# Performance work log

Hardware: AMD Instinct MI355X
Metric: run time of the kernel (lower is better)

The kernel has to match this reference:

```python
import jax, jax.numpy as jnp
import numpy as np

N, D, H = 24, 256, 8
F = D // H  # 32


def setup_inputs() -> dict:
    key = jax.random.key(0)
    ks = jax.random.split(key, 9)
    T = 8192
    x = jax.random.normal(ks[0], (T, N * D), dtype=jnp.float32)
    s = 0.02
    # Joint-specific query weights: (H, N, D, F); shared K/V: (H, D, F)
    Wq = jax.random.normal(ks[1], (H, N, D, F), dtype=jnp.float32) * s
    bq = jax.random.normal(ks[2], (H, N, F), dtype=jnp.float32) * s
    Wk = jax.random.normal(ks[3], (H, D, F), dtype=jnp.float32) * s
    bk = jax.random.normal(ks[4], (H, F), dtype=jnp.float32) * s
    Wv = jax.random.normal(ks[5], (H, D, F), dtype=jnp.float32) * s
    bv = jax.random.normal(ks[6], (H, F), dtype=jnp.float32) * s
    gamma = jnp.ones((N * D,), dtype=jnp.float32)
    beta = jnp.zeros((N * D,), dtype=jnp.float32)
    return {"x": x, "Wq": Wq, "bq": bq, "Wk": Wk, "bk": bk,
            "Wv": Wv, "bv": bv, "gamma": gamma, "beta": beta}


def reference(x, Wq, bq, Wk, bk, Wv, bv, gamma, beta):
    T = x.shape[0]
    xr = x.reshape(T, N, D)                                   # (T, N, D)
    # Shared K/V per head, joint-specific Q per head
    k = jnp.einsum('tnd,hdf->thnf', xr, Wk) + bk[None, :, None, :]
    v = jnp.einsum('tnd,hdf->thnf', xr, Wv) + bv[None, :, None, :]
    q = jnp.einsum('tnd,hndf->thnf', xr, Wq) + bq[None, :, :, :]
    scores = jnp.einsum('thnf,thmf->thnm', q, k) / jnp.sqrt(jnp.float32(F))
    attn = jax.nn.softmax(scores, axis=-1)                    # (T, H, N, N)
    out = jnp.einsum('thnm,thmf->thnf', attn, v)              # (T, H, N, F)
    # Concat heads -> (T, N, H*F) = (T, N, D)
    out = jnp.transpose(out, (0, 2, 1, 3)).reshape(T, N * D)
    # Dropout is identity in eval mode; residual + LayerNorm over N*D
    y = x + out
    mu = jnp.mean(y, axis=-1, keepdims=True)
    var = jnp.mean((y - mu) ** 2, axis=-1, keepdims=True)
    y = (y - mu) * jax.lax.rsqrt(var + 1e-5)
    return y * gamma + beta
```

## Files before the change

kernel.cpp:

```cpp
#include <hip/hip_runtime.h>

#define NT 8192
#define NJ 24
#define DD 256
#define NH 8
#define FF 32
#define C3 768

typedef __attribute__((ext_vector_type(8))) _Float16 f16x8;
typedef __attribute__((ext_vector_type(2))) _Float16 half2v;
typedef __attribute__((ext_vector_type(4))) float f32x4;

__device__ __forceinline__ unsigned short f2h(float f) {
    union { _Float16 h; unsigned short u; } c;
    c.h = (_Float16)f;
    return c.u;
}

__device__ __forceinline__ float dot2(unsigned int a, unsigned int b, float c) {
#if __has_builtin(__builtin_amdgcn_fdot2)
    return __builtin_amdgcn_fdot2(__builtin_bit_cast(half2v, a),
                                  __builtin_bit_cast(half2v, b), c, false);
#else
    half2v ha = __builtin_bit_cast(half2v, a);
    half2v hb = __builtin_bit_cast(half2v, b);
    return c + (float)ha[0] * (float)hb[0] + (float)ha[1] * (float)hb[1];
#endif
}

__device__ __forceinline__ void gload16(const void* g, void* l) {
    __builtin_amdgcn_global_load_lds(
        (const __attribute__((address_space(1))) unsigned int*)g,
        (__attribute__((address_space(3))) unsigned int*)l, 16, 0, 0);
}

__global__ __launch_bounds__(256)
void pack_wb(const float* __restrict__ Wq, const float* __restrict__ Wk,
             const float* __restrict__ Wv, unsigned short* __restrict__ wbt,
             const float* __restrict__ bq, const float* __restrict__ bk,
             const float* __restrict__ bv, float* __restrict__ bias) {
    const int b = blockIdx.x;
    const int tid = threadIdx.x;

    if (b < 208) {
        const float* src;
        int n0, nrep, crow0;
        if (b < 192) {
            int h = b / 24, n = b % 24;
            src = Wq + (size_t)(h * NJ + n) * (DD * FF);
            n0 = n; nrep = 1; crow0 = h * FF;
        } else if (b < 200) {
            int h = b - 192;
            src = Wk + (size_t)h * (DD * FF);
            n0 = 0; nrep = NJ; crow0 = 256 + h * FF;
        } else {
            int h = b - 200;
            src = Wv + (size_t)h * (DD * FF);
            n0 = 0; nrep = NJ; crow0 = 512 + h * FF;
        }
        __shared__ unsigned short T[32][264];
        #pragma unroll
        for (int it = 0; it < 4; ++it) {
            int e = (it * 256 + tid) * 8;
            int d = e >> 5;
            int f = e & 31;
            float4 v0 = *(const float4*)(src + e);
            float4 v1 = *(const float4*)(src + e + 4);
            T[f + 0][d] = f2h(v0.x); T[f + 1][d] = f2h(v0.y);
            T[f + 2][d] = f2h(v0.z); T[f + 3][d] = f2h(v0.w);
            T[f + 4][d] = f2h(v1.x); T[f + 5][d] = f2h(v1.y);
            T[f + 6][d] = f2h(v1.z); T[f + 7][d] = f2h(v1.w);
        }
        __syncthreads();
        for (int rep = 0; rep < nrep; ++rep) {
            int n = n0 + rep;
            unsigned short* dst = wbt + ((size_t)n * C3 + crow0) * DD;
            #pragma unroll
            for (int it = 0; it < 4; ++it) {
                int q = it * 256 + tid;
                int r = q >> 5;
                int c8 = (q & 31) * 8;
                *(int4*)(dst + r * DD + c8) = *(const int4*)&T[r][c8];
            }
        }
    } else {
        int idx = (b - 208) * 256 + tid;
        int cb = idx % C3;
        int nb2 = idx / C3;
        float bvv;
        if (cb < 256) {
            int h = cb >> 5, f = cb & 31;
            bvv = bq[((h * NJ + nb2) * FF) + f];
        } else if (cb < 512) {
            int cc = cb - 256; int h = cc >> 5, f = cc & 31;
            bvv = bk[h * FF + f];
        } else {
            int cc = cb - 512; int h = cc >> 5, f = cc & 31;
            bvv = bv[h * FF + f];
        }
        bias[idx] = bvv;
    }
}

#define BM 128
#define BN 128

__global__ __launch_bounds__(256, 3)
void gemm_qkv(const float* __restrict__ x, const unsigned short* __restrict__ wbt,
              const float* __restrict__ bias, unsigned short* __restrict__ qkv,
              int t0, int mbs) {
    const int nwg = gridDim.x;
    const int cpx = nwg >> 3;
    const int bid = blockIdx.x;
    const int swz = (bid & 7) * cpx + (bid >> 3);
    const int nb = swz % 6;
    const int rest = swz / 6;
    const int mb = rest % mbs;
    const int nj = rest / mbs;

    const int tid = threadIdx.x;
    const int wave = tid >> 6, lane = tid & 63;

    __shared__ unsigned short As[BM * 64];
    __shared__ unsigned short Bs[BN * 64];

    f32x4 acc[4][4];
    #pragma unroll
    for (int i = 0; i < 4; ++i)
        #pragma unroll
        for (int j = 0; j < 4; ++j)
            #pragma unroll
            for (int r = 0; r < 4; ++r) acc[i][j][r] = 0.f;

    const int trow0 = t0 + mb * BM;
    const float* srcA = x + (size_t)trow0 * (NJ * DD) + nj * DD;
    const char* srcB = (const char*)(wbt + ((size_t)nj * C3 + (size_t)nb * BN) * DD);

    const int rg = lane >> 3;
    const int sc = (lane & 7) ^ rg;

    const int wr = (wave >> 1) * 64;
    const int wc = (wave & 1) * 64;
    const int lr = lane & 15;
    const int g  = lane >> 4;

    float4 pa[4][2];
    const float* aptr[4];
    #pragma unroll
    for (int it = 0; it < 4; ++it) {
        int q = it * 256 + tid;
        int row = q >> 3;
        int c16 = q & 7;
        aptr[it] = srcA + (size_t)row * (NJ * DD) + c16 * 8;
    }

    #pragma unroll
    for (int it = 0; it < 4; ++it) {
        pa[it][0] = *(const float4*)(aptr[it]);
        pa[it][1] = *(const float4*)(aptr[it] + 4);
    }

    for (int kb = 0; kb < 4; ++kb) {
        #pragma unroll
        for (int i = 0; i < 4; ++i) {
            int row0 = wave * 32 + i * 8;
            gload16(srcB + (size_t)(row0 + rg) * (DD * 2) + kb * 128 + sc * 16,
                    (char*)Bs + row0 * 128);
        }
        #pragma unroll
        for (int it = 0; it < 4; ++it) {
            int q = it * 256 + tid;
            int row = q >> 3;
            int c16 = q & 7;
            float4 v0 = pa[it][0];
            float4 v1 = pa[it][1];
            f16x8 hv;
            hv[0] = (_Float16)v0.x; hv[1] = (_Float16)v0.y;
            hv[2] = (_Float16)v0.z; hv[3] = (_Float16)v0.w;
            hv[4] = (_Float16)v1.x; hv[5] = (_Float16)v1.y;
            hv[6] = (_Float16)v1.z; hv[7] = (_Float16)v1.w;
            int c16s = c16 ^ (row & 7);
            *(f16x8*)((char*)As + row * 128 + c16s * 16) = hv;
        }
        __syncthreads();

        if (kb < 3) {
            #pragma unroll
            for (int it = 0; it < 4; ++it) {
                const float* p = aptr[it] + (kb + 1) * 64;
                pa[it][0] = *(const float4*)p;
                pa[it][1] = *(const float4*)(p + 4);
            }
        }

        #pragma unroll
        for (int kk = 0; kk < 2; ++kk) {
            f16x8 a[4], b[4];
            #pragma unroll
            for (int i = 0; i < 4; ++i) {
                int row = wr + i * 16 + lr;
                int c16 = (kk * 4 + g) ^ (row & 7);
                a[i] = *(const f16x8*)((const char*)As + row * 128 + c16 * 16);
            }
            #pragma unroll
            for (int j = 0; j < 4; ++j) {
                int row = wc + j * 16 + lr;
                int c16 = (kk * 4 + g) ^ (row & 7);
                b[j] = *(const f16x8*)((const char*)Bs + row * 128 + c16 * 16);
            }
            #pragma unroll
            for (int i = 0; i < 4; ++i)
                #pragma unroll
                for (int j = 0; j < 4; ++j)
                    acc[i][j] = __builtin_amdgcn_mfma_f32_16x16x32_f16(a[i], b[j], acc[i][j], 0, 0, 0);
        }
        __syncthreads();
    }

    const int ln = lane & 15;
    const int lq = (lane >> 4) * 4;
    float bv[4];
    #pragma unroll
    for (int j = 0; j < 4; ++j)
        bv[j] = bias[nj * C3 + nb * BN + wc + j * 16 + ln];
    #pragma unroll
    for (int i = 0; i < 4; ++i) {
        #pragma unroll
        for (int r = 0; r < 4; ++r) {
            int trow = mb * BM + wr + i * 16 + lq + r;
            size_t base = ((size_t)trow * NJ + nj) * C3 + (size_t)nb * BN;
            #pragma unroll
            for (int j = 0; j < 4; ++j) {
                float val = acc[i][j][r] + bv[j];
                qkv[base + wc + j * 16 + ln] = f2h(val);
            }
        }
    }
}

__global__ __launch_bounds__(256, 6)
void attn_ln(const unsigned short* __restrict__ qkv, const float* __restrict__ x,
             const float* __restrict__ gamma, const float* __restrict__ beta,
             float* __restrict__ out, int t0) {
    const int tloc = blockIdx.x;
    const int t = t0 + tloc;
    const int tid = threadIdx.x;
    const int wave = tid >> 6, lane = tid & 63;

    __shared__ __align__(16) unsigned short kv[NJ * 512];
    __shared__ float red[8];
    __shared__ float stats[2];
    float4* os4 = (float4*)kv;

    const uint4* tok = (const uint4*)(qkv + (size_t)tloc * (NJ * C3));

    #pragma unroll
    for (int j = 0; j < 6; ++j) {
        int idx = tid + j * 256;
        int m = idx >> 6, r = idx & 63;
        ((uint4*)kv)[(m << 6) + r] = tok[m * 96 + 32 + r];
    }

    const bool active = tid < NH * NJ;
    const int h = active ? (tid / NJ) : 0;
    const int n = active ? (tid - h * NJ) : 0;
    unsigned int qp[16];
    if (active) {
        const uint4* qsrc = tok + n * 96 + h * 4;
        #pragma unroll
        for (int jj = 0; jj < 4; ++jj) {
            uint4 w = qsrc[jj];
            qp[jj * 4 + 0] = w.x; qp[jj * 4 + 1] = w.y;
            qp[jj * 4 + 2] = w.z; qp[jj * 4 + 3] = w.w;
        }
    }
    __syncthreads();

    half2v o2[16];
    if (active) {
        const unsigned short* kbase = kv + h * FF;
        float s[NJ];
        float mx = -1e30f;
        #pragma unroll
        for (int m = 0; m < NJ; ++m) {
            const uint4* kp = (const uint4*)(kbase + m * 512);
            float a = 0.f;
            #pragma unroll
            for (int jj = 0; jj < 4; ++jj) {
                uint4 kw = kp[jj];
                a = dot2(kw.x, qp[jj * 4 + 0], a);
                a = dot2(kw.y, qp[jj * 4 + 1], a);
                a = dot2(kw.z, qp[jj * 4 + 2], a);
                a = dot2(kw.w, qp[jj * 4 + 3], a);
            }
            a *= 0.17677669529663687f;
            s[m] = a;
            mx = fmaxf(mx, a);
        }
        float sum = 0.f;
        #pragma unroll
        for (int m = 0; m < NJ; ++m) { s[m] = __expf(s[m] - mx); sum += s[m]; }
        float inv = 1.f / sum;
        #pragma unroll
        for (int k = 0; k < 16; ++k) o2[k] = half2v{(_Float16)0.f, (_Float16)0.f};
        const unsigned short* vbase = kv + 256 + h * FF;
        #pragma unroll
        for (int m = 0; m < NJ; ++m) {
            float wm = s[m] * inv;
            half2v wv = __builtin_bit_cast(half2v, __builtin_amdgcn_cvt_pkrtz(wm, wm));
            const uint4* vp = (const uint4*)(vbase + m * 512);
            #pragma unroll
            for (int jj = 0; jj < 4; ++jj) {
                uint4 vw = vp[jj];
                o2[jj * 4 + 0] += __builtin_bit_cast(half2v, vw.x) * wv;
                o2[jj * 4 + 1] += __builtin_bit_cast(half2v, vw.y) * wv;
                o2[jj * 4 + 2] += __builtin_bit_cast(half2v, vw.z) * wv;
                o2[jj * 4 + 3] += __builtin_bit_cast(half2v, vw.w) * wv;
            }
        }
    }
    __syncthreads();
    if (active) {
        int base4 = n * 64 + h * 8;
        #pragma unroll
        for (int jj = 0; jj < 8; ++jj) {
            int wi = base4 + jj;
            int sw = wi ^ ((wi >> 6) & 7);
            os4[sw] = make_float4((float)o2[jj * 2][0], (float)o2[jj * 2][1],
                                  (float)o2[jj * 2 + 1][0], (float)o2[jj * 2 + 1][1]);
        }
    }
    __syncthreads();

    const float4* x4 = (const float4*)(x + (size_t)t * (NJ * DD));
    float4 yv[6];
    float sum = 0.f, sq = 0.f;
    #pragma unroll
    for (int j = 0; j < 6; ++j) {
        int ri = tid + j * 256;
        float4 a = x4[ri];
        float4 b = os4[ri ^ ((ri >> 6) & 7)];
        float4 y;
        y.x = a.x + b.x; y.y = a.y + b.y; y.z = a.z + b.z; y.w = a.w + b.w;
        yv[j] = y;
        sum += y.x + y.y + y.z + y.w;
        sq  += y.x * y.x + y.y * y.y + y.z * y.z + y.w * y.w;
    }
    #pragma unroll
    for (int off = 32; off > 0; off >>= 1) {
        sum += __shfl_down(sum, off);
        sq  += __shfl_down(sq, off);
    }
    if (lane == 0) { red[wave] = sum; red[4 + wave] = sq; }
    __syncthreads();
    if (tid == 0) {
        float s = red[0] + red[1] + red[2] + red[3];
        float q = red[4] + red[5] + red[6] + red[7];
        float mu = s * (1.f / 6144.f);
        float var = q * (1.f / 6144.f) - mu * mu;
        stats[0] = mu;
        stats[1] = rsqrtf(var + 1e-5f);
    }
    __syncthreads();
    const float mu = stats[0], rs = stats[1];
    const float4* g4 = (const float4*)gamma;
    const float4* b4 = (const float4*)beta;
    float4* out4 = (float4*)(out + (size_t)t * (NJ * DD));
    #pragma unroll
    for (int j = 0; j < 6; ++j) {
        float4 g = g4[tid + j * 256];
        float4 bb = b4[tid + j * 256];
        float4 y = yv[j];
        y.x = (y.x - mu) * rs * g.x + bb.x;
        y.y = (y.y - mu) * rs * g.y + bb.y;
        y.z = (y.z - mu) * rs * g.z + bb.z;
        y.w = (y.w - mu) * rs * g.w + bb.w;
        out4[tid + j * 256] = y;
    }
}

extern "C" void kernel_launch(void* const* d_in, const int* in_sizes, int n_in,
                              void* d_out, int out_size, void* d_ws, size_t ws_size,
                              hipStream_t stream) {
    const float* x     = (const float*)d_in[0];
    const float* Wq    = (const float*)d_in[1];
    const float* bq    = (const float*)d_in[2];
    const float* Wk    = (const float*)d_in[3];
    const float* bk    = (const float*)d_in[4];
    const float* Wv    = (const float*)d_in[5];
    const float* bv    = (const float*)d_in[6];
    const float* gamma = (const float*)d_in[7];
    const float* beta  = (const float*)d_in[8];
    float* out = (float*)d_out;

    char* ws = (char*)d_ws;
    const size_t wbt_bytes  = (size_t)NJ * C3 * DD * 2;
    const size_t bias_bytes = (size_t)NJ * C3 * 4;
    unsigned short* wbt = (unsigned short*)ws;
    float* bias = (float*)(ws + wbt_bytes);
    unsigned short* qkv = (unsigned short*)(ws + wbt_bytes + bias_bytes);

    const size_t fixed = wbt_bytes + bias_bytes;
    size_t avail = (ws_size > fixed) ? ws_size - fixed : 0;
    int chunk = NT;
    while (chunk > BM && (size_t)chunk * NJ * C3 * 2 > avail) chunk >>= 1;

    pack_wb<<<dim3(280), dim3(256), 0, stream>>>(Wq, Wk, Wv, wbt, bq, bk, bv, bias);

    for (int t0 = 0; t0 < NT; t0 += chunk) {
        int mbs = chunk / BM;
        gemm_qkv<<<dim3(6 * mbs * NJ), dim3(256), 0, stream>>>(x, wbt, bias, qkv, t0, mbs);
        attn_ln<<<dim3(chunk), dim3(256), 0, stream>>>(qkv, x, gamma, beta, out, t0);
    }
}
```

Measured before the change: 595.5 us.

## Double-buffer LDS tiles in QKV GEMM to overlap weight loads with MFMA

Splits the A and B shared-memory tiles into two buffers and issues the next k-step's weight loads into the alternate buffer before the current step's MFMA compute. This cuts one of the two block barriers per k-step and is meant to hide global load latency behind matrix math. It doubles LDS use per block, so launch bounds drop from 3 to 2 blocks per CU. The explicit waitcnt only covers lgkmcnt, so the direct-to-LDS loads rely on the compiler's vmcnt waits for the register prefetch to complete them.

```diff
diff --git a/kernel.cpp b/kernel.cpp
--- a/kernel.cpp
+++ b/kernel.cpp
@@ -105,7 +105,7 @@
 #define BM 128
 #define BN 128
 
-__global__ __launch_bounds__(256, 3)
+__global__ __launch_bounds__(256, 2)
 void gemm_qkv(const float* __restrict__ x, const unsigned short* __restrict__ wbt,
               const float* __restrict__ bias, unsigned short* __restrict__ qkv,
               int t0, int mbs) {
@@ -121,8 +121,8 @@
     const int tid = threadIdx.x;
     const int wave = tid >> 6, lane = tid & 63;
 
-    __shared__ unsigned short As[BM * 64];
-    __shared__ unsigned short Bs[BN * 64];
+    __shared__ unsigned short As[2][BM * 64];
+    __shared__ unsigned short Bs[2][BN * 64];
 
     f32x4 acc[4][4];
     #pragma unroll
@@ -144,7 +144,6 @@
     const int lr = lane & 15;
     const int g  = lane >> 4;
 
-    float4 pa[4][2];
     const float* aptr[4];
     #pragma unroll
     for (int it = 0; it < 4; ++it) {
@@ -155,18 +154,21 @@
     }
 
     #pragma unroll
+    for (int i = 0; i < 4; ++i) {
+        int row0 = wave * 32 + i * 8;
+        gload16(srcB + (size_t)(row0 + rg) * (DD * 2) + sc * 16,
+                (char*)Bs[0] + row0 * 128);
+    }
+    float4 pa[4][2];
+    #pragma unroll
     for (int it = 0; it < 4; ++it) {
         pa[it][0] = *(const float4*)(aptr[it]);
         pa[it][1] = *(const float4*)(aptr[it] + 4);
     }
 
+    #pragma unroll
     for (int kb = 0; kb < 4; ++kb) {
-        #pragma unroll
-        for (int i = 0; i < 4; ++i) {
-            int row0 = wave * 32 + i * 8;
-            gload16(srcB + (size_t)(row0 + rg) * (DD * 2) + kb * 128 + sc * 16,
-                    (char*)Bs + row0 * 128);
-        }
+        const int cur = kb & 1;
         #pragma unroll
         for (int it = 0; it < 4; ++it) {
             int q = it * 256 + tid;
@@ -180,11 +182,15 @@
             hv[4] = (_Float16)v1.x; hv[5] = (_Float16)v1.y;
             hv[6] = (_Float16)v1.z; hv[7] = (_Float16)v1.w;
             int c16s = c16 ^ (row & 7);
-            *(f16x8*)((char*)As + row * 128 + c16s * 16) = hv;
-        }
-        __syncthreads();
-
+            *(f16x8*)((char*)As[cur] + row * 128 + c16s * 16) = hv;
+        }
         if (kb < 3) {
+            #pragma unroll
+            for (int i = 0; i < 4; ++i) {
+                int row0 = wave * 32 + i * 8;
+                gload16(srcB + (size_t)(row0 + rg) * (DD * 2) + (kb + 1) * 128 + sc * 16,
+                        (char*)Bs[cur ^ 1] + row0 * 128);
+            }
             #pragma unroll
             for (int it = 0; it < 4; ++it) {
                 const float* p = aptr[it] + (kb + 1) * 64;
@@ -192,7 +198,9 @@
                 pa[it][1] = *(const float4*)(p + 4);
             }
         }
-
+        asm volatile("s_waitcnt lgkmcnt(0)" ::: "memory");
+        __builtin_amdgcn_sched_barrier(0);
+        __builtin_amdgcn_s_barrier();
         #pragma unroll
         for (int kk = 0; kk < 2; ++kk) {
             f16x8 a[4], b[4];
@@ -200,13 +208,13 @@
             for (int i = 0; i < 4; ++i) {
                 int row = wr + i * 16 + lr;
                 int c16 = (kk * 4 + g) ^ (row & 7);
-                a[i] = *(const f16x8*)((const char*)As + row * 128 + c16 * 16);
+                a[i] = *(const f16x8*)((const char*)As[cur] + row * 128 + c16 * 16);
             }
             #pragma unroll
             for (int j = 0; j < 4; ++j) {
                 int row = wc + j * 16 + lr;
                 int c16 = (kk * 4 + g) ^ (row & 7);
-                b[j] = *(const f16x8*)((const char*)Bs + row * 128 + c16 * 16);
+                b[j] = *(const f16x8*)((const char*)Bs[cur] + row * 128 + c16 * 16);
             }
             #pragma unroll
             for (int i = 0; i < 4; ++i)
@@ -214,7 +222,10 @@
                 for (int j = 0; j < 4; ++j)
                     acc[i][j] = __builtin_amdgcn_mfma_f32_16x16x32_f16(a[i], b[j], acc[i][j], 0, 0, 0);
         }
-        __syncthreads();
+        if (kb < 3) {
+            __builtin_amdgcn_s_barrier();
+            __builtin_amdgcn_sched_barrier(0);
+        }
     }
 
     const int ln = lane & 15;
```

After: 604.7 us. About the same (+1.5%).

## Preload full-K weight tile into LDS and read A directly from global

Applied to the files above, without the earlier changes.

The QKV GEMM now loads the entire 128x256 weight tile into shared memory once, up front, instead of per k-block, and drops the A shared-memory staging. Each wave reads its A fragments straight from global memory and converts them to fp16 in registers, which removes the per-iteration barriers. The costs are uncoalesced, duplicated global reads of x across the two column waves, a larger LDS footprint with occupancy lowered to 2, and a processing chunk reduced to 2048 rows, which adds kernel launches.

```diff
diff --git a/kernel.cpp b/kernel.cpp
--- a/kernel.cpp
+++ b/kernel.cpp
@@ -105,7 +105,7 @@
 #define BM 128
 #define BN 128
 
-__global__ __launch_bounds__(256, 3)
+__global__ __launch_bounds__(256, 2)
 void gemm_qkv(const float* __restrict__ x, const unsigned short* __restrict__ wbt,
               const float* __restrict__ bias, unsigned short* __restrict__ qkv,
               int t0, int mbs) {
@@ -121,8 +121,7 @@
     const int tid = threadIdx.x;
     const int wave = tid >> 6, lane = tid & 63;
 
-    __shared__ unsigned short As[BM * 64];
-    __shared__ unsigned short Bs[BN * 64];
+    __shared__ unsigned short Bs[BN * 256];
 
     f32x4 acc[4][4];
     #pragma unroll
@@ -135,78 +134,50 @@
     const int trow0 = t0 + mb * BM;
     const float* srcA = x + (size_t)trow0 * (NJ * DD) + nj * DD;
     const char* srcB = (const char*)(wbt + ((size_t)nj * C3 + (size_t)nb * BN) * DD);
-
-    const int rg = lane >> 3;
-    const int sc = (lane & 7) ^ rg;
 
     const int wr = (wave >> 1) * 64;
     const int wc = (wave & 1) * 64;
     const int lr = lane & 15;
     const int g  = lane >> 4;
 
-    float4 pa[4][2];
-    const float* aptr[4];
-    #pragma unroll
-    for (int it = 0; it < 4; ++it) {
-        int q = it * 256 + tid;
-        int row = q >> 3;
-        int c16 = q & 7;
-        aptr[it] = srcA + (size_t)row * (NJ * DD) + c16 * 8;
-    }
-
-    #pragma unroll
-    for (int it = 0; it < 4; ++it) {
-        pa[it][0] = *(const float4*)(aptr[it]);
-        pa[it][1] = *(const float4*)(aptr[it] + 4);
-    }
-
+    {
+        const int lcol = lane >> 5;
+        const int lg   = lane & 31;
+        #pragma unroll
+        for (int i = 0; i < 16; ++i) {
+            int c0 = wave * 32 + i * 2;
+            int col = c0 + lcol;
+            int gsrc = lg ^ (col & 7);
+            gload16(srcB + (size_t)col * 512 + gsrc * 16,
+                    (char*)Bs + c0 * 512);
+        }
+    }
+    asm volatile("s_waitcnt vmcnt(0)" ::: "memory");
+    __builtin_amdgcn_s_barrier();
+
+    #pragma unroll
     for (int kb = 0; kb < 4; ++kb) {
-        #pragma unroll
-        for (int i = 0; i < 4; ++i) {
-            int row0 = wave * 32 + i * 8;
-            gload16(srcB + (size_t)(row0 + rg) * (DD * 2) + kb * 128 + sc * 16,
-                    (char*)Bs + row0 * 128);
-        }
-        #pragma unroll
-        for (int it = 0; it < 4; ++it) {
-            int q = it * 256 + tid;
-            int row = q >> 3;
-            int c16 = q & 7;
-            float4 v0 = pa[it][0];
-            float4 v1 = pa[it][1];
-            f16x8 hv;
-            hv[0] = (_Float16)v0.x; hv[1] = (_Float16)v0.y;
-            hv[2] = (_Float16)v0.z; hv[3] = (_Float16)v0.w;
-            hv[4] = (_Float16)v1.x; hv[5] = (_Float16)v1.y;
-            hv[6] = (_Float16)v1.z; hv[7] = (_Float16)v1.w;
-            int c16s = c16 ^ (row & 7);
-            *(f16x8*)((char*)As + row * 128 + c16s * 16) = hv;
-        }
-        __syncthreads();
-
-        if (kb < 3) {
-            #pragma unroll
-            for (int it = 0; it < 4; ++it) {
-                const float* p = aptr[it] + (kb + 1) * 64;
-                pa[it][0] = *(const float4*)p;
-                pa[it][1] = *(const float4*)(p + 4);
-            }
-        }
-
         #pragma unroll
         for (int kk = 0; kk < 2; ++kk) {
             f16x8 a[4], b[4];
             #pragma unroll
             for (int i = 0; i < 4; ++i) {
-                int row = wr + i * 16 + lr;
-                int c16 = (kk * 4 + g) ^ (row & 7);
-                a[i] = *(const f16x8*)((const char*)As + row * 128 + c16 * 16);
+                const float* p = srcA + (size_t)(wr + i * 16 + lr) * (NJ * DD)
+                               + kb * 64 + kk * 32 + g * 8;
+                float4 v0 = *(const float4*)p;
+                float4 v1 = *(const float4*)(p + 4);
+                f16x8 hv;
+                hv[0] = (_Float16)v0.x; hv[1] = (_Float16)v0.y;
+                hv[2] = (_Float16)v0.z; hv[3] = (_Float16)v0.w;
+                hv[4] = (_Float16)v1.x; hv[5] = (_Float16)v1.y;
+                hv[6] = (_Float16)v1.z; hv[7] = (_Float16)v1.w;
+                a[i] = hv;
             }
             #pragma unroll
             for (int j = 0; j < 4; ++j) {
-                int row = wc + j * 16 + lr;
-                int c16 = (kk * 4 + g) ^ (row & 7);
-                b[j] = *(const f16x8*)((const char*)Bs + row * 128 + c16 * 16);
+                int col = wc + j * 16 + lr;
+                int gr = (kb * 8 + kk * 4 + g) ^ (col & 7);
+                b[j] = *(const f16x8*)((const char*)Bs + col * 512 + gr * 16);
             }
             #pragma unroll
             for (int i = 0; i < 4; ++i)
@@ -214,7 +185,6 @@
                 for (int j = 0; j < 4; ++j)
                     acc[i][j] = __builtin_amdgcn_mfma_f32_16x16x32_f16(a[i], b[j], acc[i][j], 0, 0, 0);
         }
-        __syncthreads();
     }
 
     const int ln = lane & 15;
@@ -402,7 +372,7 @@
 
     const size_t fixed = wbt_bytes + bias_bytes;
     size_t avail = (ws_size > fixed) ? ws_size - fixed : 0;
-    int chunk = NT;
+    int chunk = 2048;
     while (chunk > BM && (size_t)chunk * NJ * C3 * 2 > avail) chunk >>= 1;
 
     pack_wb<<<dim3(280), dim3(256), 0, stream>>>(Wq, Wk, Wv, wbt, bq, bk, bv, bias);
```

Result: slower. 804.3 us (+35.1%).
